# Optimization experiments

Hardware: AMD Instinct MI355X
Metric: run time of the kernel (lower is better)

Reference implementation:

```python
import jax, jax.numpy as jnp
import numpy as np

H = 51  # hidden size hardcoded in the module


def _lstm_cell(x, h, c, W_ih, b_ih, W_hh, b_hh):
    # PyTorch LSTMCell: gates in i, f, g, o order
    gates = x @ W_ih.T + b_ih + h @ W_hh.T + b_hh  # [B, 4H]
    i, f, g, o = jnp.split(gates, 4, axis=-1)
    i = jax.nn.sigmoid(i)
    f = jax.nn.sigmoid(f)
    g = jnp.tanh(g)
    o = jax.nn.sigmoid(o)
    c_new = f * c + i * g
    h_new = o * jnp.tanh(c_new)
    return h_new, c_new


def setup_inputs() -> dict:
    key = jax.random.key(0)
    ks = jax.random.split(key, 12)
    B, T = 2048, 256
    s1 = 1.0 / np.sqrt(H)
    u = lambda k, shape: jax.random.uniform(k, shape, jnp.float32, -s1, s1)
    return {
        "inputs": jax.random.normal(ks[0], (B, T), jnp.float32),
        "W_ih1": u(ks[1], (4 * H, 1)),
        "b_ih1": u(ks[2], (4 * H,)),
        "W_hh1": u(ks[3], (4 * H, H)),
        "b_hh1": u(ks[4], (4 * H,)),
        "W_ih2": u(ks[5], (4 * H, H)),
        "b_ih2": u(ks[6], (4 * H,)),
        "W_hh2": u(ks[7], (4 * H, H)),
        "b_hh2": u(ks[8], (4 * H,)),
        "W_lin": u(ks[9], (1, H)),
        "b_lin": u(ks[10], (1,)),
        "future": 16,
    }


def reference(inputs, W_ih1, b_ih1, W_hh1, b_hh1, W_ih2, b_ih2, W_hh2, b_hh2,
              W_lin, b_lin, future):
    B, T = inputs.shape
    h1 = jnp.zeros((B, H), inputs.dtype)
    c1 = jnp.zeros((B, H), inputs.dtype)
    h2 = jnp.zeros((B, H), inputs.dtype)
    c2 = jnp.zeros((B, H), inputs.dtype)

    def core(x_t, h1, c1, h2, c2):
        h1, c1 = _lstm_cell(x_t, h1, c1, W_ih1, b_ih1, W_hh1, b_hh1)
        h2, c2 = _lstm_cell(h1, h2, c2, W_ih2, b_ih2, W_hh2, b_hh2)
        out = h2 @ W_lin.T + b_lin  # [B, 1]
        return out, h1, c1, h2, c2

    def step(carry, x_t):
        h1, c1, h2, c2, _ = carry
        out, h1, c1, h2, c2 = core(x_t, h1, c1, h2, c2)
        return (h1, c1, h2, c2, out), out

    xs = inputs.T[:, :, None]  # [T, B, 1]
    init_out = jnp.zeros((B, 1), inputs.dtype)
    carry, outs_seen = jax.lax.scan(step, (h1, c1, h2, c2, init_out), xs)

    def fstep(carry, _):
        h1, c1, h2, c2, out = carry
        out, h1, c1, h2, c2 = core(out, h1, c1, h2, c2)
        return (h1, c1, h2, c2, out), out

    if future > 0:
        _, outs_fut = jax.lax.scan(fstep, carry, None, length=future)
        outs = jnp.concatenate([outs_seen, outs_fut], axis=0)  # [T+F, B, 1]
    else:
        outs = outs_seen
    return outs[:, :, 0].T  # [B, T+future]
```

## Files before the change

kernel.cpp:

```cpp
#include <hip/hip_runtime.h>
#include <math.h>

#define H 51
#define TSEEN 256
#define FUT 16
#define TTOT (TSEEN + FUT)
#define NB 8
#define THREADS 512
#define NWAVE 8
#define UPW 7
#define NBLOCKS (2048 / NB)

typedef _Float16 f16;
typedef _Float16 f16x8 __attribute__((ext_vector_type(8)));
typedef float f32x4 __attribute__((ext_vector_type(4)));

__device__ __forceinline__ float fast_rcp(float x) { return __builtin_amdgcn_rcpf(x); }
__device__ __forceinline__ float sigf(float x) {
  return fast_rcp(1.f + __expf(-x));
}
__device__ __forceinline__ float tanhf_(float x) {
  return fmaf(2.f, fast_rcp(1.f + __expf(-2.f * x)), -1.f);
}

__device__ __forceinline__ float xor8f(float v) {
  return __int_as_float(__builtin_amdgcn_mov_dpp(__float_as_int(v), 0x128, 0xf, 0xf, true));
}

#define MFMA __builtin_amdgcn_mfma_f32_16x16x32_f16

__launch_bounds__(THREADS, 2)
__global__ void lstm2_kernel(const float* __restrict__ inp,
                             const float* __restrict__ Wih1,
                             const float* __restrict__ bih1,
                             const float* __restrict__ Whh1,
                             const float* __restrict__ bhh1,
                             const float* __restrict__ Wih2,
                             const float* __restrict__ bih2,
                             const float* __restrict__ Whh2,
                             const float* __restrict__ bhh2,
                             const float* __restrict__ Wlin,
                             const float* __restrict__ blin,
                             float* __restrict__ out)
{
  __shared__ __align__(16) f16 Bh1[2][2][64][8];
  __shared__ __align__(16) f16 Bh2[2][2][64][8];
  __shared__ __align__(16) float xs[TSEEN][NB];
  __shared__ float parts[2][NWAVE][NB];
  __shared__ float outb[TTOT][NB];

  const int tid  = threadIdx.x;
  const int wv   = tid >> 6;
  const int lane = tid & 63;
  const int l15  = lane & 15;
  const int g4   = lane >> 4;
  const int bq   = l15 & 7;
  const bool mhi = (l15 & 8) != 0;
  const int baseb = blockIdx.x * NB;

  {
    f16* b1 = &Bh1[0][0][0][0];
    f16* b2 = &Bh2[0][0][0][0];
    for (int i = tid; i < 2 * 2 * 64 * 8; i += THREADS) {
      b1[i] = (f16)0.f; b2[i] = (f16)0.f;
    }
  }
  for (int i = tid; i < NB * TSEEN; i += THREADS) {
    int b = i >> 8, t = i & 255;
    xs[t][b] = inp[(size_t)(baseb + b) * TSEEN + t];
  }
  if (tid < 2 * NWAVE * NB) (&parts[0][0][0])[tid] = 0.f;

  f16x8 A1[2][2], A2[2][2], A3[2][2];
  #pragma unroll
  for (int m = 0; m < 2; ++m) {
    const int slotA = 4 * m + (l15 >> 2);
    const int uA = UPW * wv + slotA;
    const int gA = l15 & 3;
    const bool vA = (slotA < UPW) && (uA < H);
    const int row = gA * H + (vA ? uA : 0);
    #pragma unroll
    for (int kt = 0; kt < 2; ++kt) {
      #pragma unroll
      for (int j = 0; j < 8; ++j) {
        const int k = 32 * kt + 8 * g4 + j;
        float w1 = 0.f, w2 = 0.f, w3 = 0.f;
        if (vA) {
          if (k < H) {
            w1 = Whh1[row * H + k];
            w2 = Wih2[row * H + k];
            w3 = Whh2[row * H + k];
          } else if (k == H) {
            w1 = Wih1[row];
          }
        }
        A1[m][kt][j] = (f16)w1;
        A2[m][kt][j] = (f16)w2;
        A3[m][kt][j] = (f16)w3;
      }
    }
  }

  f32x4 bias1[2], bias2[2];
  #pragma unroll
  for (int m = 0; m < 2; ++m) {
    const int ulC = 4 * m + g4;
    const int u = UPW * wv + ulC;
    const bool v = (ulC < UPW) && (u < H) && (l15 < 8);
    #pragma unroll
    for (int r = 0; r < 4; ++r) {
      const int rr = r * H + (v ? u : 0);
      bias1[m][r] = v ? (bih1[rr] + bhh1[rr]) : 0.f;
      bias2[m][r] = v ? (bih2[rr] + bhh2[rr]) : 0.f;
    }
  }

  const int slotC = (mhi ? 4 : 0) + g4;
  const int uC0 = UPW * wv + slotC;
  const bool vC = (slotC < UPW) && (uC0 < H);
  const int uC = vC ? uC0 : 0;
  const float wl = vC ? Wlin[uC] : 0.f;
  const float bl = blin[0];
  const int wkt = uC >> 5;
  const int wln = bq + 16 * ((uC >> 3) & 3);
  const int wj  = uC & 7;

  float c1 = 0.f, c2 = 0.f;

  __syncthreads();
  if (tid < NB) {
    float x0 = xs[0][tid];
    f16 xh = (f16)x0;
    Bh1[1][1][tid + 32][3] = xh;
    Bh1[1][1][tid + 40][3] = (f16)(x0 - (float)xh);
  }
  __syncthreads();

  #pragma unroll 1
  for (int t = 0; t < TTOT; ++t) {
    const int pw = t & 1, pr = pw ^ 1;

    const f16x8 b1k0 = *(const f16x8*)&Bh1[pr][0][lane][0];
    const f16x8 b1k1 = *(const f16x8*)&Bh1[pr][1][lane][0];

    f32x4 ac1[2];
    #pragma unroll
    for (int m = 0; m < 2; ++m) {
      f32x4 c = MFMA(A1[m][0], b1k0, bias1[m], 0, 0, 0);
      ac1[m] = MFMA(A1[m][1], b1k1, c, 0, 0, 0);
    }

    float q0, q1, q2, q3;
    {
      float s00 = ac1[0][0] + xor8f(ac1[0][0]);
      float s01 = ac1[0][1] + xor8f(ac1[0][1]);
      float s02 = ac1[0][2] + xor8f(ac1[0][2]);
      float s03 = ac1[0][3] + xor8f(ac1[0][3]);
      float s10 = ac1[1][0] + xor8f(ac1[1][0]);
      float s11 = ac1[1][1] + xor8f(ac1[1][1]);
      float s12 = ac1[1][2] + xor8f(ac1[1][2]);
      float s13 = ac1[1][3] + xor8f(ac1[1][3]);
      q0 = mhi ? s10 : s00;
      q1 = mhi ? s11 : s01;
      q2 = mhi ? s12 : s02;
      q3 = mhi ? s13 : s03;
    }
    {
      float iv = sigf(q0), fv = sigf(q1);
      float gv = tanhf_(q2), ov = sigf(q3);
      c1 = fmaf(fv, c1, iv * gv);
      float h1n = ov * tanhf_(c1);
      if (vC) {
        f16 hh = (f16)h1n;
        Bh1[pw][wkt][wln][wj]     = hh;
        Bh1[pw][wkt][wln + 8][wj] = (f16)(h1n - (float)hh);
      }
    }
    if (t + 1 < TSEEN && tid < NB) {
      float xn = xs[t + 1][tid];
      f16 xh = (f16)xn;
      Bh1[pw][1][tid + 32][3] = xh;
      Bh1[pw][1][tid + 40][3] = (f16)(xn - (float)xh);
    }
    __syncthreads();

    if (t >= 1 && t < TSEEN && tid < NB) {
      float s = bl;
      #pragma unroll
      for (int w = 0; w < NWAVE; ++w) s += parts[pr][w][tid];
      outb[t - 1][tid] = s;
    }

    const f16x8 b2k0 = *(const f16x8*)&Bh2[pr][0][lane][0];
    const f16x8 b2k1 = *(const f16x8*)&Bh2[pr][1][lane][0];
    const f16x8 f1k0 = *(const f16x8*)&Bh1[pw][0][lane][0];
    const f16x8 f1k1 = *(const f16x8*)&Bh1[pw][1][lane][0];

    f32x4 ac2[2];
    #pragma unroll
    for (int m = 0; m < 2; ++m) {
      f32x4 c = MFMA(A3[m][0], b2k0, bias2[m], 0, 0, 0);
      c = MFMA(A3[m][1], b2k1, c, 0, 0, 0);
      c = MFMA(A2[m][0], f1k0, c, 0, 0, 0);
      ac2[m] = MFMA(A2[m][1], f1k1, c, 0, 0, 0);
    }

    {
      float s00 = ac2[0][0] + xor8f(ac2[0][0]);
      float s01 = ac2[0][1] + xor8f(ac2[0][1]);
      float s02 = ac2[0][2] + xor8f(ac2[0][2]);
      float s03 = ac2[0][3] + xor8f(ac2[0][3]);
      float s10 = ac2[1][0] + xor8f(ac2[1][0]);
      float s11 = ac2[1][1] + xor8f(ac2[1][1]);
      float s12 = ac2[1][2] + xor8f(ac2[1][2]);
      float s13 = ac2[1][3] + xor8f(ac2[1][3]);
      q0 = mhi ? s10 : s00;
      q1 = mhi ? s11 : s01;
      q2 = mhi ? s12 : s02;
      q3 = mhi ? s13 : s03;
    }
    float pv;
    {
      float iv = sigf(q0), fv = sigf(q1);
      float gv = tanhf_(q2), ov = sigf(q3);
      c2 = fmaf(fv, c2, iv * gv);
      float h2n = ov * tanhf_(c2);
      pv = wl * h2n;
      if (vC) {
        f16 hh = (f16)h2n;
        Bh2[pw][wkt][wln][wj]     = hh;
        Bh2[pw][wkt][wln + 8][wj] = (f16)(h2n - (float)hh);
      }
    }
    pv += xor8f(pv);
    pv += __shfl_xor(pv, 16, 64);
    pv += __shfl_xor(pv, 32, 64);
    if (lane < NB) parts[pw][wv][lane] = pv;

    if (t >= TSEEN - 1) {
      __syncthreads();
      if (tid < NB) {
        float fbv = bl;
        #pragma unroll
        for (int w = 0; w < NWAVE; ++w) fbv += parts[pw][w][tid];
        outb[t][tid] = fbv;
        if (t < TTOT - 1) {
          f16 xh = (f16)fbv;
          Bh1[pw][1][tid + 32][3] = xh;
          Bh1[pw][1][tid + 40][3] = (f16)(fbv - (float)xh);
        }
      }
      __syncthreads();
    }
  }

  __syncthreads();
  for (int i = tid; i < TTOT * NB; i += THREADS) {
    int b = i / TTOT, t = i - b * TTOT;
    out[(size_t)(baseb + b) * TTOT + t] = outb[t][b];
  }
}

extern "C" void kernel_launch(void* const* d_in, const int* in_sizes, int n_in,
                              void* d_out, int out_size, void* d_ws, size_t ws_size,
                              hipStream_t stream) {
  (void)in_sizes; (void)n_in; (void)d_ws; (void)ws_size; (void)out_size;
  const float* inp  = (const float*)d_in[0];
  const float* Wih1 = (const float*)d_in[1];
  const float* bih1 = (const float*)d_in[2];
  const float* Whh1 = (const float*)d_in[3];
  const float* bhh1 = (const float*)d_in[4];
  const float* Wih2 = (const float*)d_in[5];
  const float* bih2 = (const float*)d_in[6];
  const float* Whh2 = (const float*)d_in[7];
  const float* bhh2 = (const float*)d_in[8];
  const float* Wlin = (const float*)d_in[9];
  const float* blin = (const float*)d_in[10];
  float* outp = (float*)d_out;

  lstm2_kernel<<<NBLOCKS, THREADS, 0, stream>>>(
      inp, Wih1, bih1, Whh1, bhh1, Wih2, bih2, Whh2, bhh2, Wlin, blin, outp);
}
```

Measured before the change: 232.6 us.

## Hoist next-step layer-1 MFMA into layer-2 phase and halve DPP recombine

```diff
diff --git a/kernel.cpp b/kernel.cpp
--- a/kernel.cpp
+++ b/kernel.cpp
@@ -28,6 +28,22 @@
 }
 
 #define MFMA __builtin_amdgcn_mfma_f32_16x16x32_f16
+
+__device__ __forceinline__ void recomb(const f32x4& a0, const f32x4& a1, bool mhi,
+                                       float& q0, float& q1, float& q2, float& q3) {
+  float s0 = mhi ? a0[0] : a1[0];
+  float s1 = mhi ? a0[1] : a1[1];
+  float s2 = mhi ? a0[2] : a1[2];
+  float s3 = mhi ? a0[3] : a1[3];
+  float k0 = mhi ? a1[0] : a0[0];
+  float k1 = mhi ? a1[1] : a0[1];
+  float k2 = mhi ? a1[2] : a0[2];
+  float k3 = mhi ? a1[3] : a0[3];
+  q0 = k0 + xor8f(s0);
+  q1 = k1 + xor8f(s1);
+  q2 = k2 + xor8f(s2);
+  q3 = k3 + xor8f(s3);
+}
 
 __launch_bounds__(THREADS, 2)
 __global__ void lstm2_kernel(const float* __restrict__ inp,
@@ -126,6 +142,7 @@
   const int wj  = uC & 7;
 
   float c1 = 0.f, c2 = 0.f;
+  const f32x4 zf = {0.f, 0.f, 0.f, 0.f};
 
   __syncthreads();
   if (tid < NB) {
@@ -136,35 +153,23 @@
   }
   __syncthreads();
 
+  f32x4 ac1[2];
+  {
+    const f16x8 p0 = *(const f16x8*)&Bh1[1][0][lane][0];
+    const f16x8 p1 = *(const f16x8*)&Bh1[1][1][lane][0];
+    #pragma unroll
+    for (int m = 0; m < 2; ++m) {
+      f32x4 c = MFMA(A1[m][0], p0, bias1[m], 0, 0, 0);
+      ac1[m] = MFMA(A1[m][1], p1, c, 0, 0, 0);
+    }
+  }
+
   #pragma unroll 1
   for (int t = 0; t < TTOT; ++t) {
     const int pw = t & 1, pr = pw ^ 1;
 
-    const f16x8 b1k0 = *(const f16x8*)&Bh1[pr][0][lane][0];
-    const f16x8 b1k1 = *(const f16x8*)&Bh1[pr][1][lane][0];
-
-    f32x4 ac1[2];
-    #pragma unroll
-    for (int m = 0; m < 2; ++m) {
-      f32x4 c = MFMA(A1[m][0], b1k0, bias1[m], 0, 0, 0);
-      ac1[m] = MFMA(A1[m][1], b1k1, c, 0, 0, 0);
-    }
-
     float q0, q1, q2, q3;
-    {
-      float s00 = ac1[0][0] + xor8f(ac1[0][0]);
-      float s01 = ac1[0][1] + xor8f(ac1[0][1]);
-      float s02 = ac1[0][2] + xor8f(ac1[0][2]);
-      float s03 = ac1[0][3] + xor8f(ac1[0][3]);
-      float s10 = ac1[1][0] + xor8f(ac1[1][0]);
-      float s11 = ac1[1][1] + xor8f(ac1[1][1]);
-      float s12 = ac1[1][2] + xor8f(ac1[1][2]);
-      float s13 = ac1[1][3] + xor8f(ac1[1][3]);
-      q0 = mhi ? s10 : s00;
-      q1 = mhi ? s11 : s01;
-      q2 = mhi ? s12 : s02;
-      q3 = mhi ? s13 : s03;
-    }
+    recomb(ac1[0], ac1[1], mhi, q0, q1, q2, q3);
     {
       float iv = sigf(q0), fv = sigf(q1);
       float gv = tanhf_(q2), ov = sigf(q3);
@@ -199,26 +204,16 @@
     f32x4 ac2[2];
     #pragma unroll
     for (int m = 0; m < 2; ++m) {
-      f32x4 c = MFMA(A3[m][0], b2k0, bias2[m], 0, 0, 0);
-      c = MFMA(A3[m][1], b2k1, c, 0, 0, 0);
-      c = MFMA(A2[m][0], f1k0, c, 0, 0, 0);
-      ac2[m] = MFMA(A2[m][1], f1k1, c, 0, 0, 0);
-    }
-
-    {
-      float s00 = ac2[0][0] + xor8f(ac2[0][0]);
-      float s01 = ac2[0][1] + xor8f(ac2[0][1]);
-      float s02 = ac2[0][2] + xor8f(ac2[0][2]);
-      float s03 = ac2[0][3] + xor8f(ac2[0][3]);
-      float s10 = ac2[1][0] + xor8f(ac2[1][0]);
-      float s11 = ac2[1][1] + xor8f(ac2[1][1]);
-      float s12 = ac2[1][2] + xor8f(ac2[1][2]);
-      float s13 = ac2[1][3] + xor8f(ac2[1][3]);
-      q0 = mhi ? s10 : s00;
-      q1 = mhi ? s11 : s01;
-      q2 = mhi ? s12 : s02;
-      q3 = mhi ? s13 : s03;
-    }
+      f32x4 r1 = MFMA(A3[m][0], b2k0, bias2[m], 0, 0, 0);
+      r1 = MFMA(A3[m][1], b2k1, r1, 0, 0, 0);
+      f32x4 r2 = MFMA(A2[m][0], f1k0, zf, 0, 0, 0);
+      r2 = MFMA(A2[m][1], f1k1, r2, 0, 0, 0);
+      ac2[m] = r1 + r2;
+      f32x4 n = MFMA(A1[m][0], f1k0, bias1[m], 0, 0, 0);
+      ac1[m] = MFMA(A1[m][1], f1k1, n, 0, 0, 0);
+    }
+
+    recomb(ac2[0], ac2[1], mhi, q0, q1, q2, q3);
     float pv;
     {
       float iv = sigf(q0), fv = sigf(q1);
@@ -251,6 +246,15 @@
         }
       }
       __syncthreads();
+      if (t < TTOT - 1) {
+        const f16x8 g0 = *(const f16x8*)&Bh1[pw][0][lane][0];
+        const f16x8 g1 = *(const f16x8*)&Bh1[pw][1][lane][0];
+        #pragma unroll
+        for (int m = 0; m < 2; ++m) {
+          f32x4 c = MFMA(A1[m][0], g0, bias1[m], 0, 0, 0);
+          ac1[m] = MFMA(A1[m][1], g1, c, 0, 0, 0);
+        }
+      }
     }
   }
 
```

Measured after the change: 231.0 us. Within noise of the previous version (-0.7%).
